# Performance work log

Measured on AMD Instinct MI355X. Metric: run time of the kernel, lower is better.

## Reference

```python
import jax, jax.numpy as jnp
import numpy as np

NHID = 512
NCLS = 250
CHUNK = 200  # words per class (equal class_chunks), vocab = NCLS*CHUNK = 50000
N = 2048     # flattened tokens (batch*seq after masking)


def setup_inputs() -> dict:
    key = jax.random.key(0)
    k1, k2, k3, k4, k5 = jax.random.split(key, 5)
    r = 0.1  # init_weights uniform range
    x = jax.random.normal(k1, (N, NHID), dtype=jnp.float32)
    cls_idx = jax.random.randint(k2, (N,), 0, NCLS, dtype=jnp.int64)
    Wc = jax.random.uniform(k3, (NCLS, NHID), jnp.float32, -r, r)   # cls_decoder.weight
    bc = jnp.zeros((NCLS,), jnp.float32)                             # cls_decoder.bias
    Ww = jax.random.uniform(k4, (NCLS, CHUNK, NHID), jnp.float32, -r, r)  # stacked words_decoders weights
    bw = jnp.zeros((NCLS, CHUNK), jnp.float32)                       # stacked words_decoders biases
    return {"x": x, "Wc": Wc, "bc": bc, "Ww": Ww, "bw": bw, "cls_idx": cls_idx}


def reference(x, Wc, bc, Ww, bw, cls_idx):
    # Class logits for every token: cls_decoder(input)
    p_class = jnp.einsum('nh,ch->nc', x, Wc) + bc          # [N, NCLS]
    # Per-class word decoders: each token goes through the Linear of its class.
    # Equivalent to the dict-based index_select + per-class Linear in the
    # original forward (rows reordered per-token instead of grouped by class).
    Wg = Ww[cls_idx]                                       # [N, CHUNK, NHID] irregular gather
    bg = bw[cls_idx]                                       # [N, CHUNK]
    p_words = jnp.einsum('nkh,nh->nk', Wg, x) + bg         # [N, CHUNK]
    # Concatenate class and within-class logits into one array output.
    return jnp.concatenate([p_class, p_words], axis=1)     # [N, NCLS+CHUNK]
```

## Files before the change

kernel.cpp:

```cpp
#include <hip/hip_runtime.h>

#define NHID   512
#define NCLS   250
#define CHUNK  200
#define NTOK   2048
#define NOUT   450
#define MAXTOK 32
#define NTHR   256

#define CLS_UNITS 512
#define WRD_UNITS (NCLS * 8)
#define NUNITS    (CLS_UNITS + WRD_UNITS)
#define NBLK      ((NUNITS + 3) / 4)

typedef __attribute__((ext_vector_type(8))) short bf16x8;
typedef __attribute__((ext_vector_type(4))) float f32x4;

__global__ void scatter_kernel(const int* __restrict__ cls_idx,
                               int* __restrict__ cnt, int* __restrict__ list) {
    int i = blockIdx.x * blockDim.x + threadIdx.x;
    if (i < NTOK) {
        int c = cls_idx[i];
        int p = atomicAdd(&cnt[c], 1);
        if (p < MAXTOK) list[c * MAXTOK + p] = i;
    }
}

__device__ __forceinline__ unsigned hpack(unsigned a, unsigned b) {
    return __builtin_amdgcn_perm(a, b, 0x07060302u);
}

__device__ __forceinline__ void cvt8(float4 va, float4 vb, bf16x8& h, bf16x8& l) {
    unsigned u0 = __float_as_uint(va.x), u1 = __float_as_uint(va.y);
    unsigned u2 = __float_as_uint(va.z), u3 = __float_as_uint(va.w);
    unsigned u4 = __float_as_uint(vb.x), u5 = __float_as_uint(vb.y);
    unsigned u6 = __float_as_uint(vb.z), u7 = __float_as_uint(vb.w);
    union { unsigned w[4]; bf16x8 v; } H, L;
    H.w[0] = hpack(u1, u0); H.w[1] = hpack(u3, u2);
    H.w[2] = hpack(u5, u4); H.w[3] = hpack(u7, u6);
    float r0 = va.x - __uint_as_float(u0 & 0xffff0000u);
    float r1 = va.y - __uint_as_float(u1 & 0xffff0000u);
    float r2 = va.z - __uint_as_float(u2 & 0xffff0000u);
    float r3 = va.w - __uint_as_float(u3 & 0xffff0000u);
    float r4 = vb.x - __uint_as_float(u4 & 0xffff0000u);
    float r5 = vb.y - __uint_as_float(u5 & 0xffff0000u);
    float r6 = vb.z - __uint_as_float(u6 & 0xffff0000u);
    float r7 = vb.w - __uint_as_float(u7 & 0xffff0000u);
    L.w[0] = hpack(__float_as_uint(r1), __float_as_uint(r0));
    L.w[1] = hpack(__float_as_uint(r3), __float_as_uint(r2));
    L.w[2] = hpack(__float_as_uint(r5), __float_as_uint(r4));
    L.w[3] = hpack(__float_as_uint(r7), __float_as_uint(r6));
    h = H.v; l = L.v;
}

template <int NK>
__device__ __forceinline__ void ktile(const float* __restrict__ ap,
                                      const float* const* bp, f32x4* acc) {
    #pragma unroll 2
    for (int s = 0; s < 16; ++s) {
        float4 a0 = *(const float4*)(ap + s * 32);
        float4 a1 = *(const float4*)(ap + s * 32 + 4);
        bf16x8 ah, al;
        cvt8(a0, a1, ah, al);
        #pragma unroll
        for (int k = 0; k < NK; ++k) {
            float4 b0 = *(const float4*)(bp[k] + s * 32);
            float4 b1 = *(const float4*)(bp[k] + s * 32 + 4);
            bf16x8 bh, bl;
            cvt8(b0, b1, bh, bl);
            acc[k] = __builtin_amdgcn_mfma_f32_16x16x32_bf16(ah, bh, acc[k], 0, 0, 0);
            acc[k] = __builtin_amdgcn_mfma_f32_16x16x32_bf16(al, bh, acc[k], 0, 0, 0);
            acc[k] = __builtin_amdgcn_mfma_f32_16x16x32_bf16(ah, bl, acc[k], 0, 0, 0);
        }
    }
}

__global__ __launch_bounds__(NTHR, 2)
void cbd_mfma(const float* __restrict__ x,  const float* __restrict__ Wc,
              const float* __restrict__ bc, const float* __restrict__ Ww,
              const float* __restrict__ bw, const int* __restrict__ cnt_ws,
              const int* __restrict__ list_ws, float* __restrict__ out)
{
    const int unit = blockIdx.x * 4 + (threadIdx.x >> 6);
    if (unit >= NUNITS) return;
    const int l = threadIdx.x & 63;
    const int n = l & 15;
    const int q = l >> 4;

    const bool is_cls = unit < CLS_UNITS;
    int c = 0, mtile, ntg, count = NTOK;
    if (is_cls) {
        mtile = unit >> 2;
        ntg   = unit & 3;
    } else {
        int v = unit - CLS_UNITS;
        c     = v >> 3;
        int t = v & 7;
        mtile = t >> 2;
        ntg   = t & 3;
        count = cnt_ws[c];
        if (count > MAXTOK) count = MAXTOK;
        if (mtile * 16 >= count) return;
    }

    int tokA, tokS[4];
    bool sval[4];
    if (is_cls) {
        tokA = mtile * 16 + n;
        #pragma unroll
        for (int i = 0; i < 4; ++i) { tokS[i] = mtile * 16 + q * 4 + i; sval[i] = true; }
    } else {
        int mi = mtile * 16 + n;
        tokA = list_ws[c * MAXTOK + (mi < count ? mi : count - 1)];
        #pragma unroll
        for (int i = 0; i < 4; ++i) {
            int m = mtile * 16 + q * 4 + i;
            sval[i] = m < count;
            tokS[i] = list_ws[c * MAXTOK + (sval[i] ? m : count - 1)];
        }
    }
    const float* ap = x + (size_t)tokA * NHID + q * 8;

    const float* bp[4];
    float bias[4];
    int   col[4];
    bool  rv[4];
    #pragma unroll
    for (int k = 0; k < 4; ++k) {
        int r = (ntg * 4 + k) * 16 + n;
        if (is_cls) {
            rv[k] = r < NCLS;
            int rc = rv[k] ? r : NCLS - 1;
            bp[k]   = Wc + (size_t)rc * NHID + q * 8;
            bias[k] = bc[rc];
            col[k]  = rc;
        } else {
            rv[k] = r < CHUNK;
            int rc = rv[k] ? r : CHUNK - 1;
            bp[k]   = Ww + ((size_t)c * CHUNK + rc) * NHID + q * 8;
            bias[k] = bw[c * CHUNK + rc];
            col[k]  = NCLS + rc;
        }
    }

    f32x4 acc[4] = {{0,0,0,0},{0,0,0,0},{0,0,0,0},{0,0,0,0}};
    const bool full = is_cls || (ntg < 3);
    if (full) ktile<4>(ap, bp, acc);
    else      ktile<1>(ap, bp, acc);

    const int nk = full ? 4 : 1;
    #pragma unroll
    for (int k = 0; k < 4; ++k) {
        if (k < nk && rv[k]) {
            #pragma unroll
            for (int i = 0; i < 4; ++i) {
                if (sval[i])
                    out[(size_t)tokS[i] * NOUT + col[k]] = acc[k][i] + bias[k];
            }
        }
    }
}

extern "C" void kernel_launch(void* const* d_in, const int* in_sizes, int n_in,
                              void* d_out, int out_size, void* d_ws, size_t ws_size,
                              hipStream_t stream) {
    const float* x   = (const float*)d_in[0];
    const float* Wc  = (const float*)d_in[1];
    const float* bc  = (const float*)d_in[2];
    const float* Ww  = (const float*)d_in[3];
    const float* bw  = (const float*)d_in[4];
    const int*   cls = (const int*)d_in[5];
    float* out = (float*)d_out;

    int* cnt  = (int*)d_ws;
    int* list = cnt + 256;

    hipMemsetAsync(cnt, 0, 256 * sizeof(int), stream);
    hipLaunchKernelGGL(scatter_kernel, dim3((NTOK + 255) / 256), dim3(256),
                       0, stream, cls, cnt, list);
    hipLaunchKernelGGL(cbd_mfma, dim3(NBLK), dim3(NTHR), 0, stream,
                       x, Wc, bc, Ww, bw, cnt, list, out);
}
```

Baseline: 200.9 us.

## Narrow per-wave tiles to two column groups, loop over token tiles, add register prefetch

Each wave now computes two 16-column groups instead of four. Word units cover all of a class's tokens in an inner loop over 16-token tiles, so one class uses seven units rather than eight. The K loop is rewritten with a three-stage register software pipeline that issues loads for later steps while the current step converts and runs MFMAs. The aim is to hide global load latency, spread work across more waves, and drop the idle word units. The cost is that each wave reloads the activation rows for every pair of column groups, and classes with two token tiles now run them one after the other in a single wave.

```diff
diff --git a/kernel.cpp b/kernel.cpp
--- a/kernel.cpp
+++ b/kernel.cpp
@@ -8,8 +8,8 @@
 #define MAXTOK 32
 #define NTHR   256
 
-#define CLS_UNITS 512
-#define WRD_UNITS (NCLS * 8)
+#define CLS_UNITS 1024
+#define WRD_UNITS (NCLS * 7)
 #define NUNITS    (CLS_UNITS + WRD_UNITS)
 #define NBLK      ((NUNITS + 3) / 4)
 
@@ -53,28 +53,6 @@
     h = H.v; l = L.v;
 }
 
-template <int NK>
-__device__ __forceinline__ void ktile(const float* __restrict__ ap,
-                                      const float* const* bp, f32x4* acc) {
-    #pragma unroll 2
-    for (int s = 0; s < 16; ++s) {
-        float4 a0 = *(const float4*)(ap + s * 32);
-        float4 a1 = *(const float4*)(ap + s * 32 + 4);
-        bf16x8 ah, al;
-        cvt8(a0, a1, ah, al);
-        #pragma unroll
-        for (int k = 0; k < NK; ++k) {
-            float4 b0 = *(const float4*)(bp[k] + s * 32);
-            float4 b1 = *(const float4*)(bp[k] + s * 32 + 4);
-            bf16x8 bh, bl;
-            cvt8(b0, b1, bh, bl);
-            acc[k] = __builtin_amdgcn_mfma_f32_16x16x32_bf16(ah, bh, acc[k], 0, 0, 0);
-            acc[k] = __builtin_amdgcn_mfma_f32_16x16x32_bf16(al, bh, acc[k], 0, 0, 0);
-            acc[k] = __builtin_amdgcn_mfma_f32_16x16x32_bf16(ah, bl, acc[k], 0, 0, 0);
-        }
-    }
-}
-
 __global__ __launch_bounds__(NTHR, 2)
 void cbd_mfma(const float* __restrict__ x,  const float* __restrict__ Wc,
               const float* __restrict__ bc, const float* __restrict__ Ww,
@@ -88,74 +66,106 @@
     const int q = l >> 4;
 
     const bool is_cls = unit < CLS_UNITS;
-    int c = 0, mtile, ntg, count = NTOK;
+    int c = 0, ntp, m0 = 0, mlim, count = 0;
     if (is_cls) {
-        mtile = unit >> 2;
-        ntg   = unit & 3;
+        int mtile = unit >> 3;
+        ntp  = unit & 7;
+        m0   = mtile * 16;
+        mlim = m0 + 16;
     } else {
         int v = unit - CLS_UNITS;
-        c     = v >> 3;
-        int t = v & 7;
-        mtile = t >> 2;
-        ntg   = t & 3;
+        c   = v / 7;
+        ntp = v % 7;
         count = cnt_ws[c];
+        if (count <= 0) return;
         if (count > MAXTOK) count = MAXTOK;
-        if (mtile * 16 >= count) return;
+        mlim = count;
     }
 
-    int tokA, tokS[4];
-    bool sval[4];
+    const int r0 = (2 * ntp) * 16 + n;
+    const int r1 = r0 + 16;
+    bool rv0, rv1; int col0, col1; float bias0, bias1;
+    const float *bpt0, *bpt1;
     if (is_cls) {
-        tokA = mtile * 16 + n;
-        #pragma unroll
-        for (int i = 0; i < 4; ++i) { tokS[i] = mtile * 16 + q * 4 + i; sval[i] = true; }
+        rv0 = r0 < NCLS; rv1 = r1 < NCLS;
+        int rc0 = rv0 ? r0 : NCLS - 1, rc1 = rv1 ? r1 : NCLS - 1;
+        bpt0 = Wc + (size_t)rc0 * NHID + q * 8;
+        bpt1 = Wc + (size_t)rc1 * NHID + q * 8;
+        bias0 = bc[rc0]; bias1 = bc[rc1];
+        col0 = rc0; col1 = rc1;
     } else {
-        int mi = mtile * 16 + n;
-        tokA = list_ws[c * MAXTOK + (mi < count ? mi : count - 1)];
+        rv0 = r0 < CHUNK; rv1 = r1 < CHUNK;
+        int rc0 = rv0 ? r0 : CHUNK - 1, rc1 = rv1 ? r1 : CHUNK - 1;
+        bpt0 = Ww + ((size_t)c * CHUNK + rc0) * NHID + q * 8;
+        bpt1 = Ww + ((size_t)c * CHUNK + rc1) * NHID + q * 8;
+        bias0 = bw[c * CHUNK + rc0]; bias1 = bw[c * CHUNK + rc1];
+        col0 = NCLS + rc0; col1 = NCLS + rc1;
+    }
+
+    for (int mbase = m0; mbase < mlim; mbase += 16) {
+        int tokA, tokS[4]; bool sv[4];
+        if (is_cls) {
+            tokA = mbase + n;
+            #pragma unroll
+            for (int i = 0; i < 4; ++i) { tokS[i] = mbase + q * 4 + i; sv[i] = true; }
+        } else {
+            int mi = mbase + n;
+            tokA = list_ws[c * MAXTOK + (mi < count ? mi : count - 1)];
+            #pragma unroll
+            for (int i = 0; i < 4; ++i) {
+                int m = mbase + q * 4 + i;
+                sv[i]   = m < count;
+                tokS[i] = list_ws[c * MAXTOK + (sv[i] ? m : count - 1)];
+            }
+        }
+        const float* ap = x + (size_t)tokA * NHID + q * 8;
+
+        f32x4 acc0 = {0.f, 0.f, 0.f, 0.f};
+        f32x4 acc1 = {0.f, 0.f, 0.f, 0.f};
+
+        float4 Pa0,Pa1,Pb0,Pb1,Pc0,Pc1;
+        float4 Qa0,Qa1,Qb0,Qb1,Qc0,Qc1;
+        float4 Ra0,Ra1,Rb0,Rb1,Rc0,Rc1;
+
+#define LDR(S, A0,A1,B0,B1,C0,C1) {                                          \
+        int _s = (S) < 16 ? (S) : 15;                                        \
+        const float* _a = ap   + _s * 32;                                    \
+        const float* _b = bpt0 + _s * 32;                                    \
+        const float* _c = bpt1 + _s * 32;                                    \
+        A0 = *(const float4*)_a; A1 = *(const float4*)(_a + 4);              \
+        B0 = *(const float4*)_b; B1 = *(const float4*)(_b + 4);              \
+        C0 = *(const float4*)_c; C1 = *(const float4*)(_c + 4); }
+
+#define CMPR(A0,A1,B0,B1,C0,C1) {                                            \
+        bf16x8 ah, al, bh, bl;                                               \
+        cvt8(A0, A1, ah, al);                                                \
+        cvt8(B0, B1, bh, bl);                                                \
+        acc0 = __builtin_amdgcn_mfma_f32_16x16x32_bf16(ah, bh, acc0, 0,0,0); \
+        acc0 = __builtin_amdgcn_mfma_f32_16x16x32_bf16(al, bh, acc0, 0,0,0); \
+        acc0 = __builtin_amdgcn_mfma_f32_16x16x32_bf16(ah, bl, acc0, 0,0,0); \
+        cvt8(C0, C1, bh, bl);                                                \
+        acc1 = __builtin_amdgcn_mfma_f32_16x16x32_bf16(ah, bh, acc1, 0,0,0); \
+        acc1 = __builtin_amdgcn_mfma_f32_16x16x32_bf16(al, bh, acc1, 0,0,0); \
+        acc1 = __builtin_amdgcn_mfma_f32_16x16x32_bf16(ah, bl, acc1, 0,0,0); }
+
+        LDR(0, Pa0,Pa1,Pb0,Pb1,Pc0,Pc1);
+        LDR(1, Qa0,Qa1,Qb0,Qb1,Qc0,Qc1);
+        LDR(2, Ra0,Ra1,Rb0,Rb1,Rc0,Rc1);
+        for (int s = 0; s < 15; s += 3) {
+            CMPR(Pa0,Pa1,Pb0,Pb1,Pc0,Pc1);  LDR(s + 3, Pa0,Pa1,Pb0,Pb1,Pc0,Pc1);
+            CMPR(Qa0,Qa1,Qb0,Qb1,Qc0,Qc1);  LDR(s + 4, Qa0,Qa1,Qb0,Qb1,Qc0,Qc1);
+            CMPR(Ra0,Ra1,Rb0,Rb1,Rc0,Rc1);  LDR(s + 5, Ra0,Ra1,Rb0,Rb1,Rc0,Rc1);
+        }
+        CMPR(Pa0,Pa1,Pb0,Pb1,Pc0,Pc1);
+#undef LDR
+#undef CMPR
+
         #pragma unroll
         for (int i = 0; i < 4; ++i) {
-            int m = mtile * 16 + q * 4 + i;
-            sval[i] = m < count;
-            tokS[i] = list_ws[c * MAXTOK + (sval[i] ? m : count - 1)];
-        }
-    }
-    const float* ap = x + (size_t)tokA * NHID + q * 8;
-
-    const float* bp[4];
-    float bias[4];
-    int   col[4];
-    bool  rv[4];
-    #pragma unroll
-    for (int k = 0; k < 4; ++k) {
-        int r = (ntg * 4 + k) * 16 + n;
-        if (is_cls) {
-            rv[k] = r < NCLS;
-            int rc = rv[k] ? r : NCLS - 1;
-            bp[k]   = Wc + (size_t)rc * NHID + q * 8;
-            bias[k] = bc[rc];
-            col[k]  = rc;
-        } else {
-            rv[k] = r < CHUNK;
-            int rc = rv[k] ? r : CHUNK - 1;
-            bp[k]   = Ww + ((size_t)c * CHUNK + rc) * NHID + q * 8;
-            bias[k] = bw[c * CHUNK + rc];
-            col[k]  = NCLS + rc;
-        }
-    }
-
-    f32x4 acc[4] = {{0,0,0,0},{0,0,0,0},{0,0,0,0},{0,0,0,0}};
-    const bool full = is_cls || (ntg < 3);
-    if (full) ktile<4>(ap, bp, acc);
-    else      ktile<1>(ap, bp, acc);
-
-    const int nk = full ? 4 : 1;
-    #pragma unroll
-    for (int k = 0; k < 4; ++k) {
-        if (k < nk && rv[k]) {
-            #pragma unroll
-            for (int i = 0; i < 4; ++i) {
-                if (sval[i])
-                    out[(size_t)tokS[i] * NOUT + col[k]] = acc[k][i] + bias[k];
+            if (sv[i]) {
+                size_t ro = (size_t)tokS[i] * NOUT;
+                if (rv0) out[ro + col0] = acc0[i] + bias0;
+                if (rv1) out[ro + col1] = acc1[i] + bias1;
             }
         }
     }
```

Result: slower. 235.9 us (+17.4%).

## Fuse scatter and decoders into one kernel with async LDS weight staging

Applied to the files above, without the earlier changes.

Drops the memset and the separate scatter launch. Each block now rebuilds the token list for its class from cls_idx using ballots. One wave per class streams that class's word-decoder weights into LDS through double-buffered global_load_lds, while a second wave in the block computes a class-decoder tile. A few extra blocks use an LDS histogram to pick up overflow tokens for classes with more than 16 tokens. This trades many small waves for few long-running ones, so per-wave latency and the low number of in-flight waves may limit throughput. Overflow handling is capped by the 8 spare blocks, which risks dropped outputs if many classes exceed 16 tokens.

```diff
diff --git a/kernel.cpp b/kernel.cpp
--- a/kernel.cpp
+++ b/kernel.cpp
@@ -5,26 +5,14 @@
 #define CHUNK  200
 #define NTOK   2048
 #define NOUT   450
+#define NTHR   128
+#define NBLK   258
 #define MAXTOK 32
-#define NTHR   256
-
-#define CLS_UNITS 512
-#define WRD_UNITS (NCLS * 8)
-#define NUNITS    (CLS_UNITS + WRD_UNITS)
-#define NBLK      ((NUNITS + 3) / 4)
 
 typedef __attribute__((ext_vector_type(8))) short bf16x8;
 typedef __attribute__((ext_vector_type(4))) float f32x4;
 
-__global__ void scatter_kernel(const int* __restrict__ cls_idx,
-                               int* __restrict__ cnt, int* __restrict__ list) {
-    int i = blockIdx.x * blockDim.x + threadIdx.x;
-    if (i < NTOK) {
-        int c = cls_idx[i];
-        int p = atomicAdd(&cnt[c], 1);
-        if (p < MAXTOK) list[c * MAXTOK + p] = i;
-    }
-}
+#define MFMA(a, b, c) __builtin_amdgcn_mfma_f32_16x16x32_bf16((a), (b), (c), 0, 0, 0)
 
 __device__ __forceinline__ unsigned hpack(unsigned a, unsigned b) {
     return __builtin_amdgcn_perm(a, b, 0x07060302u);
@@ -53,110 +41,217 @@
     h = H.v; l = L.v;
 }
 
-template <int NK>
-__device__ __forceinline__ void ktile(const float* __restrict__ ap,
-                                      const float* const* bp, f32x4* acc) {
-    #pragma unroll 2
-    for (int s = 0; s < 16; ++s) {
-        float4 a0 = *(const float4*)(ap + s * 32);
-        float4 a1 = *(const float4*)(ap + s * 32 + 4);
-        bf16x8 ah, al;
-        cvt8(a0, a1, ah, al);
-        #pragma unroll
-        for (int k = 0; k < NK; ++k) {
-            float4 b0 = *(const float4*)(bp[k] + s * 32);
-            float4 b1 = *(const float4*)(bp[k] + s * 32 + 4);
-            bf16x8 bh, bl;
-            cvt8(b0, b1, bh, bl);
-            acc[k] = __builtin_amdgcn_mfma_f32_16x16x32_bf16(ah, bh, acc[k], 0, 0, 0);
-            acc[k] = __builtin_amdgcn_mfma_f32_16x16x32_bf16(al, bh, acc[k], 0, 0, 0);
-            acc[k] = __builtin_amdgcn_mfma_f32_16x16x32_bf16(ah, bl, acc[k], 0, 0, 0);
-        }
-    }
-}
-
-__global__ __launch_bounds__(NTHR, 2)
-void cbd_mfma(const float* __restrict__ x,  const float* __restrict__ Wc,
-              const float* __restrict__ bc, const float* __restrict__ Ww,
-              const float* __restrict__ bw, const int* __restrict__ cnt_ws,
-              const int* __restrict__ list_ws, float* __restrict__ out)
+__device__ __forceinline__ void async16(const float* g, float* lds_base) {
+    __builtin_amdgcn_global_load_lds(
+        (const __attribute__((address_space(1))) unsigned*)g,
+        (__attribute__((address_space(3))) unsigned*)lds_base, 16, 0, 0);
+}
+
+__device__ __forceinline__ void lds_fence_wave() {
+    __builtin_amdgcn_wave_barrier();
+    asm volatile("s_waitcnt lgkmcnt(0)" ::: "memory");
+    __builtin_amdgcn_wave_barrier();
+}
+
+__global__ __launch_bounds__(NTHR, 1)
+void cbd_fused(const float* __restrict__ x,  const float* __restrict__ Wc,
+               const float* __restrict__ bc, const float* __restrict__ Ww,
+               const float* __restrict__ bw, const int* __restrict__ cls_idx,
+               float* __restrict__ out)
 {
-    const int unit = blockIdx.x * 4 + (threadIdx.x >> 6);
-    if (unit >= NUNITS) return;
-    const int l = threadIdx.x & 63;
-    const int n = l & 15;
-    const int q = l >> 4;
-
-    const bool is_cls = unit < CLS_UNITS;
-    int c = 0, mtile, ntg, count = NTOK;
-    if (is_cls) {
-        mtile = unit >> 2;
-        ntg   = unit & 3;
+    __shared__ short Afrag[2][16 * 64 * 8];
+    __shared__ float Bbuf[2][16 * 256];
+
+    const int bid  = blockIdx.x;
+    const int tid  = threadIdx.x;
+    const int wid  = tid >> 6;
+    const int lane = tid & 63;
+    const int n    = lane & 15;
+    const int q    = lane >> 4;
+
+    if (wid == 1) {
+        if (bid < 256) {
+            const int mt = bid >> 1, hn = bid & 1;
+            const float* ap = x + (size_t)(mt * 16 + n) * NHID + q * 8;
+            #pragma unroll
+            for (int g4 = 0; g4 < 2; ++g4) {
+                const float* bp[4]; float bias[4]; int col[4]; bool rv[4];
+                #pragma unroll
+                for (int k = 0; k < 4; ++k) {
+                    int r = (hn * 8 + g4 * 4 + k) * 16 + n;
+                    rv[k] = r < NCLS;
+                    int rc = rv[k] ? r : NCLS - 1;
+                    bp[k]   = Wc + (size_t)rc * NHID + q * 8;
+                    bias[k] = bc[rc];
+                    col[k]  = rc;
+                }
+                f32x4 acc[4] = {{0,0,0,0},{0,0,0,0},{0,0,0,0},{0,0,0,0}};
+                #pragma unroll 2
+                for (int s = 0; s < 16; ++s) {
+                    float4 a0 = *(const float4*)(ap + s * 32);
+                    float4 a1 = *(const float4*)(ap + s * 32 + 4);
+                    bf16x8 ah, al; cvt8(a0, a1, ah, al);
+                    #pragma unroll
+                    for (int k = 0; k < 4; ++k) {
+                        float4 b0 = *(const float4*)(bp[k] + s * 32);
+                        float4 b1 = *(const float4*)(bp[k] + s * 32 + 4);
+                        bf16x8 bh, bl; cvt8(b0, b1, bh, bl);
+                        acc[k] = MFMA(ah, bh, acc[k]);
+                        acc[k] = MFMA(al, bh, acc[k]);
+                        acc[k] = MFMA(ah, bl, acc[k]);
+                    }
+                }
+                #pragma unroll
+                for (int k = 0; k < 4; ++k)
+                    if (rv[k]) {
+                        #pragma unroll
+                        for (int i = 0; i < 4; ++i)
+                            out[(size_t)(mt * 16 + q * 4 + i) * NOUT + col[k]]
+                                = acc[k][i] + bias[k];
+                    }
+            }
+        }
+        return;
+    }
+
+    int myvals[32];
+    #pragma unroll
+    for (int it = 0; it < 8; ++it) {
+        int4 v = *(const int4*)&cls_idx[it * 256 + lane * 4];
+        myvals[it*4+0] = v.x; myvals[it*4+1] = v.y;
+        myvals[it*4+2] = v.z; myvals[it*4+3] = v.w;
+    }
+
+    int c, slotbase;
+    const float* wsrc;
+    bool issued01 = false;
+    if (bid < NCLS) {
+        c = bid; slotbase = 0;
+        wsrc = Ww + (size_t)c * CHUNK * NHID;
+        #pragma unroll
+        for (int r = 0; r < 16; ++r)
+            async16(wsrc + (size_t)r * NHID + lane * 4, &Bbuf[0][r * 256]);
+        #pragma unroll
+        for (int r = 0; r < 16; ++r)
+            async16(wsrc + (size_t)r * NHID + 256 + lane * 4, &Bbuf[1][r * 256]);
+        issued01 = true;
     } else {
-        int v = unit - CLS_UNITS;
-        c     = v >> 3;
-        int t = v & 7;
-        mtile = t >> 2;
-        ntg   = t & 3;
-        count = cnt_ws[c];
-        if (count > MAXTOK) count = MAXTOK;
-        if (mtile * 16 >= count) return;
-    }
-
-    int tokA, tokS[4];
-    bool sval[4];
-    if (is_cls) {
-        tokA = mtile * 16 + n;
-        #pragma unroll
-        for (int i = 0; i < 4; ++i) { tokS[i] = mtile * 16 + q * 4 + i; sval[i] = true; }
-    } else {
-        int mi = mtile * 16 + n;
-        tokA = list_ws[c * MAXTOK + (mi < count ? mi : count - 1)];
-        #pragma unroll
-        for (int i = 0; i < 4; ++i) {
-            int m = mtile * 16 + q * 4 + i;
-            sval[i] = m < count;
-            tokS[i] = list_ws[c * MAXTOK + (sval[i] ? m : count - 1)];
-        }
-    }
-    const float* ap = x + (size_t)tokA * NHID + q * 8;
-
-    const float* bp[4];
-    float bias[4];
-    int   col[4];
-    bool  rv[4];
+        int* hist = (int*)&Bbuf[0][0];
+        for (int i = lane; i < 256; i += 64) hist[i] = 0;
+        lds_fence_wave();
+        #pragma unroll
+        for (int j = 0; j < 32; ++j) atomicAdd(&hist[myvals[j]], 1);
+        lds_fence_wave();
+        int kk = bid - NCLS, found = -1, runbase = 0;
+        #pragma unroll
+        for (int ch = 0; ch < 4; ++ch) {
+            int hv = hist[ch * 64 + lane];
+            unsigned long long m = __ballot(hv > 16);
+            int c2 = (int)__popcll(m);
+            if (found < 0 && kk < runbase + c2) {
+                unsigned long long mm = m;
+                for (int t = 0; t < 8; ++t) if (t < kk - runbase) mm &= mm - 1;
+                found = ch * 64 + (__ffsll((long long)mm) - 1);
+            }
+            runbase += c2;
+        }
+        if (found < 0) return;
+        c = found; slotbase = 16;
+        wsrc = Ww + (size_t)c * CHUNK * NHID;
+    }
+
+    int* toktmp = (int*)&Afrag[0][0];
+    int cnt = 0;
     #pragma unroll
-    for (int k = 0; k < 4; ++k) {
-        int r = (ntg * 4 + k) * 16 + n;
-        if (is_cls) {
-            rv[k] = r < NCLS;
-            int rc = rv[k] ? r : NCLS - 1;
-            bp[k]   = Wc + (size_t)rc * NHID + q * 8;
-            bias[k] = bc[rc];
-            col[k]  = rc;
-        } else {
-            rv[k] = r < CHUNK;
-            int rc = rv[k] ? r : CHUNK - 1;
-            bp[k]   = Ww + ((size_t)c * CHUNK + rc) * NHID + q * 8;
-            bias[k] = bw[c * CHUNK + rc];
-            col[k]  = NCLS + rc;
-        }
-    }
-
-    f32x4 acc[4] = {{0,0,0,0},{0,0,0,0},{0,0,0,0},{0,0,0,0}};
-    const bool full = is_cls || (ntg < 3);
-    if (full) ktile<4>(ap, bp, acc);
-    else      ktile<1>(ap, bp, acc);
-
-    const int nk = full ? 4 : 1;
+    for (int j = 0; j < 32; ++j) {
+        int idx  = (j >> 2) * 256 + lane * 4 + (j & 3);
+        bool hit = (myvals[j] == c);
+        unsigned long long m = __ballot(hit);
+        if (hit) {
+            int pos = cnt + (int)__popcll(m & ((1ull << lane) - 1ull));
+            if (pos < MAXTOK) toktmp[pos] = idx;
+        }
+        cnt += (int)__popcll(m);
+    }
+    const int cntc = cnt < MAXTOK ? cnt : MAXTOK;
+    if (slotbase >= cntc || cntc == 0) {
+        if (issued01) asm volatile("s_waitcnt vmcnt(0)" ::: "memory");
+        return;
+    }
+    lds_fence_wave();
+    int idx_slot = slotbase + n;
+    int mytokr   = toktmp[idx_slot < cntc ? idx_slot : 0];
+    lds_fence_wave();
+
+    if (!issued01) {
+        #pragma unroll
+        for (int r = 0; r < 16; ++r)
+            async16(wsrc + (size_t)r * NHID + lane * 4, &Bbuf[0][r * 256]);
+        #pragma unroll
+        for (int r = 0; r < 16; ++r)
+            async16(wsrc + (size_t)r * NHID + 256 + lane * 4, &Bbuf[1][r * 256]);
+    }
+
+    int tkS[4]; bool msk[4];
     #pragma unroll
-    for (int k = 0; k < 4; ++k) {
-        if (k < nk && rv[k]) {
-            #pragma unroll
-            for (int i = 0; i < 4; ++i) {
-                if (sval[i])
-                    out[(size_t)tokS[i] * NOUT + col[k]] = acc[k][i] + bias[k];
+    for (int i = 0; i < 4; ++i) {
+        int ml = q * 4 + i;
+        tkS[i] = __shfl(mytokr, ml);
+        msk[i] = (slotbase + ml) < cntc;
+    }
+
+    {
+        int tk = __shfl(mytokr, n);
+        #pragma unroll
+        for (int it = 0; it < 16; ++it) {
+            const float* xp = x + (size_t)tk * NHID + it * 32 + q * 8;
+            float4 va = *(const float4*)xp, vb = *(const float4*)(xp + 4);
+            bf16x8 hh, ll; cvt8(va, vb, hh, ll);
+            int u = it * 64 + lane;
+            *(bf16x8*)&Afrag[0][u * 8] = hh;
+            *(bf16x8*)&Afrag[1][u * 8] = ll;
+        }
+    }
+    lds_fence_wave();
+
+    f32x4 acc = {0.f, 0.f, 0.f, 0.f};
+    for (int hp = 0; hp < 26; ++hp) {
+        const int p = hp >> 1, h = hp & 1, buf = hp & 1;
+        asm volatile("s_waitcnt vmcnt(0)" ::: "memory");
+        __builtin_amdgcn_wave_barrier();
+
+        if (h == 0) { acc[0] = 0.f; acc[1] = 0.f; acc[2] = 0.f; acc[3] = 0.f; }
+        #pragma unroll
+        for (int ss = 0; ss < 8; ++ss) {
+            const int sg = h * 8 + ss;
+            bf16x8 ah = *(const bf16x8*)&Afrag[0][(sg * 64 + lane) * 8];
+            bf16x8 al = *(const bf16x8*)&Afrag[1][(sg * 64 + lane) * 8];
+            const float* bq = &Bbuf[buf][n * 256 + ss * 32 + q * 8];
+            float4 b0 = *(const float4*)bq;
+            float4 b1 = *(const float4*)(bq + 4);
+            bf16x8 bh, bl; cvt8(b0, b1, bh, bl);
+            acc = MFMA(ah, bh, acc);
+            acc = MFMA(al, bh, acc);
+            acc = MFMA(ah, bl, acc);
+        }
+
+        if (h == 1) {
+            int r = p * 16 + n;
+            if (r < CHUNK) {
+                float bias = bw[c * CHUNK + r];
+                #pragma unroll
+                for (int i = 0; i < 4; ++i)
+                    if (msk[i])
+                        out[(size_t)tkS[i] * NOUT + NCLS + r] = acc[i] + bias;
             }
+        }
+
+        if (hp + 2 < 26) {
+            const int p2 = (hp + 2) >> 1, h2 = (hp + 2) & 1;
+            const int nrow = (p2 == 12) ? 8 : 16;
+            const float* base = wsrc + (size_t)(p2 * 16) * NHID + h2 * 256 + lane * 4;
+            for (int r = 0; r < nrow; ++r)
+                async16(base + (size_t)r * NHID, &Bbuf[buf][r * 256]);
         }
     }
 }
@@ -171,13 +266,6 @@
     const float* bw  = (const float*)d_in[4];
     const int*   cls = (const int*)d_in[5];
     float* out = (float*)d_out;
-
-    int* cnt  = (int*)d_ws;
-    int* list = cnt + 256;
-
-    hipMemsetAsync(cnt, 0, 256 * sizeof(int), stream);
-    hipLaunchKernelGGL(scatter_kernel, dim3((NTOK + 255) / 256), dim3(256),
-                       0, stream, cls, cnt, list);
-    hipLaunchKernelGGL(cbd_mfma, dim3(NBLK), dim3(NTHR), 0, stream,
-                       x, Wc, bc, Ww, bw, cnt, list, out);
-}
+    hipLaunchKernelGGL(cbd_fused, dim3(NBLK), dim3(NTHR), 0, stream,
+                       x, Wc, bc, Ww, bw, cls, out);
+}
```

After: 190.6 us. 5.1% less time.
